# Performance work log

Measured on AMD Instinct MI355X. Metric: run time of the kernel, lower is better.

The kernel has to match this reference:

```python
import jax, jax.numpy as jnp
import numpy as np

B, T, HID = 2, 1024, 2048
H, DK, DV = 16, 128, 128
KC = 4          # short-conv kernel size
CHUNK = 64
EPS = 1e-5


def _dwconv_silu(x, w):
    # causal depthwise conv1d + SiLU: x [B,T,C], w [C,K]
    K = w.shape[1]
    xp = jnp.pad(x, ((0, 0), (K - 1, 0), (0, 0)))
    y = sum(xp[:, i:i + x.shape[1], :] * w[:, i] for i in range(K))
    return jax.nn.silu(y)


def _l2norm(x):
    return x * jax.lax.rsqrt(jnp.sum(x * x, -1, keepdims=True) + 1e-6)


def setup_inputs() -> dict:
    key = jax.random.key(0)
    ks = jax.random.split(key, 22)
    std = 0.02
    w = lambda k, s: jax.random.normal(k, s, jnp.float32) * std
    return dict(
        hidden_states=jax.random.normal(ks[0], (B, T, HID), jnp.float32),
        Wq=w(ks[1], (HID, H * DK)),
        Wk=w(ks[2], (HID, H * DK)),
        Wv=w(ks[3], (HID, H * DV)),
        conv_wq=w(ks[4], (H * DK, KC)),
        conv_wk=w(ks[5], (H * DK, KC)),
        conv_wv=w(ks[6], (H * DV, KC)),
        Wgb1=w(ks[7], (HID, DV)), Wgb2=w(ks[8], (DV, H * DK)),
        Wgd1=w(ks[9], (HID, DV)), Wgd2=w(ks[10], (DV, H * DK)),
        Wbb=w(ks[11], (HID, H)), Wbd=w(ks[12], (HID, H)),
        Wlam=w(ks[13], (HID, H)),
        A_log=jnp.log(jax.random.uniform(ks[14], (H,), jnp.float32, 1.0, 16.0)),
        dt_bias=jnp.zeros((H * DK,), jnp.float32),
        Wg1=w(ks[15], (HID, DV)), Wg2=w(ks[16], (DV, H * DV)),
        bg2=jnp.zeros((H * DV,), jnp.float32),
        onorm_w=jnp.ones((DV,), jnp.float32),
        Wo=w(ks[17], (H * DV, HID)),
    )


def _fkda_core(q, k, v, gf, gs, bf, bs):
    # dual-state (fast/slow) gated delta rule.
    # q,k: [B,T,H,DK]; v: [B,T,H,DV]; gf/gs: log-decay [B,T,H,DK]; bf/bs: [B,T,H]
    scale = DK ** -0.5
    tm = lambda x: jnp.moveaxis(x, 1, 0)                 # time-major
    qT, kT, vT = tm(q) * scale, tm(k), tm(v)
    g2 = jnp.stack([tm(gf), tm(gs)], 1)                  # [T,2,B,H,DK]
    b2 = jnp.stack([tm(bf), tm(bs)], 1)                  # [T,2,B,H]
    NC = T // CHUNK
    chunkify = lambda x: x.reshape((NC, CHUNK) + x.shape[1:])
    inputs = tuple(map(chunkify, (qT, kT, vT, g2, b2)))

    def step(S, inp):
        qt, kt, vt, gt, bt = inp                         # S: [2,B,H,DK,DV]
        S = S * jnp.exp(gt)[..., None]                   # per-channel decay on key dim
        mem = jnp.einsum('bhk,sbhkv->sbhv', kt, S)       # current memory readout
        u = bt[..., None] * (vt[None] - mem)             # delta-rule residual write
        S = S + jnp.einsum('bhk,sbhv->sbhkv', kt, u)
        o = jnp.einsum('bhk,sbhkv->sbhv', qt, S)
        return S, o

    @jax.checkpoint
    def chunk_step(S, inp):
        return jax.lax.scan(step, S, inp)

    S0 = jnp.zeros((2, q.shape[0], H, DK, DV), q.dtype)
    _, o = jax.lax.scan(chunk_step, S0, inputs)          # [NC,CHUNK,2,B,H,DV]
    o = o.reshape((T,) + o.shape[2:])
    return jnp.moveaxis(o[:, 0], 0, 1), jnp.moveaxis(o[:, 1], 0, 1)


def reference(hidden_states, Wq, Wk, Wv, conv_wq, conv_wk, conv_wv,
              Wgb1, Wgb2, Wgd1, Wgd2, Wbb, Wbd, Wlam, A_log, dt_bias,
              Wg1, Wg2, bg2, onorm_w, Wo):
    x = hidden_states
    b, t, _ = x.shape
    q = _dwconv_silu(x @ Wq, conv_wq).reshape(b, t, H, DK)
    k = _dwconv_silu(x @ Wk, conv_wk).reshape(b, t, H, DK)
    v = _dwconv_silu(x @ Wv, conv_wv).reshape(b, t, H, DV)
    g_base = ((x @ Wgb1) @ Wgb2).reshape(b, t, H, DK)    # low-rank decay gates
    g_delta = ((x @ Wgd1) @ Wgd2).reshape(b, t, H, DK)
    bb, bd = x @ Wbb, x @ Wbd
    lam = jax.nn.sigmoid(x @ Wlam)                       # [b,t,H] fast/slow mix
    beta_fast = jax.nn.sigmoid(bb + bd)
    beta_slow = jax.nn.sigmoid(bb - bd)
    dtb = dt_bias.reshape(H, DK)
    gate_of = lambda g: -jnp.exp(A_log)[None, None, :, None] * jax.nn.softplus(g + dtb)
    gf = gate_of(g_base + g_delta)                       # fused_kda_gate, fast
    gs = gate_of(g_base - g_delta)                       # slow (share_decay_gate=False)
    q, k = _l2norm(q), _l2norm(k)                        # use_qk_l2norm_in_kernel
    o_f, o_s = _fkda_core(q, k, v, gf, gs, beta_fast, beta_slow)
    o = lam[..., None] * o_f + (1.0 - lam[..., None]) * o_s
    gate = ((x @ Wg1) @ Wg2 + bg2).reshape(b, t, H, DV)
    o = o * jax.lax.rsqrt(jnp.mean(o * o, -1, keepdims=True) + EPS) * onorm_w
    o = o * jax.nn.sigmoid(gate)                         # FusedRMSNormGated(sigmoid)
    return o.reshape(b, t, H * DV) @ Wo
```

## Files before the change

kernel.cpp:

```cpp
#include <hip/hip_runtime.h>
#include <hip/hip_bf16.h>
#include <math.h>
#include <stdint.h>

#define B_   2
#define T_   1024
#define HID_ 2048
#define H_   16
#define DK_  128
#define DV_  128
#define TS_  16

typedef __bf16 bf16;
typedef __attribute__((ext_vector_type(8))) __bf16 bf16x8;
typedef __attribute__((ext_vector_type(4))) float f32x4;

typedef __attribute__((address_space(3))) uint32_t* lds_ptr_t;
typedef const __attribute__((address_space(1))) uint32_t* glb_ptr_t;

__device__ __forceinline__ float sigmoidf_(float x) {
    return 1.0f / (1.0f + __expf(-x));
}

__device__ __forceinline__ void ldg_to_lds16(const void* g, void* lds) {
    __builtin_amdgcn_global_load_lds((glb_ptr_t)(uintptr_t)g,
                                     (lds_ptr_t)(uintptr_t)lds, 16, 0, 0);
}

template <int CTRL>
__device__ __forceinline__ float dpp_ror_add(float x) {
    int yi = __builtin_amdgcn_update_dpp(
        0, __builtin_bit_cast(int, x), CTRL, 0xF, 0xF, true);
    return x + __builtin_bit_cast(float, yi);
}
__device__ __forceinline__ float row16_allreduce(float x) {
    x = dpp_ror_add<0x128>(x);
    x = dpp_ror_add<0x124>(x);
    x = dpp_ror_add<0x122>(x);
    x = dpp_ror_add<0x121>(x);
    return x;
}

__global__ __launch_bounds__(256) void cast_bf16_kernel(
    const float* __restrict__ in, bf16* __restrict__ out)
{
    int i = blockIdx.x * 256 + threadIdx.x;
    float4 a = ((const float4*)in)[2 * i];
    float4 b = ((const float4*)in)[2 * i + 1];
    bf16x8 o;
    o[0] = (bf16)a.x; o[1] = (bf16)a.y; o[2] = (bf16)a.z; o[3] = (bf16)a.w;
    o[4] = (bf16)b.x; o[5] = (bf16)b.y; o[6] = (bf16)b.z; o[7] = (bf16)b.w;
    ((bf16x8*)out)[i] = o;
}

__global__ __launch_bounds__(256) void tcast_kernel(
    const float* __restrict__ W, bf16* __restrict__ Wt, int K, int N)
{
    __shared__ float tile[32][33];
    const int k0 = blockIdx.y * 32, n0 = blockIdx.x * 32;
    const int r = threadIdx.x >> 5, c = threadIdx.x & 31;
    #pragma unroll
    for (int i = 0; i < 4; ++i)
        tile[r + 8 * i][c] = W[(size_t)(k0 + r + 8 * i) * N + n0 + c];
    __syncthreads();
    #pragma unroll
    for (int i = 0; i < 4; ++i)
        Wt[(size_t)(n0 + r + 8 * i) * K + k0 + c] = (bf16)tile[c][r + 8 * i];
}

__global__ __launch_bounds__(256) void mfma_gemm_kernel(
    const bf16* __restrict__ A, const bf16* __restrict__ Bt,
    const float* __restrict__ bias, void* __restrict__ Cout,
    int M, int N, int Kfull, int lda, int ldc, int ksplit, int bf16out)
{
    __shared__ bf16 As[128 * 32];
    __shared__ bf16 Bs[128 * 32];

    const int tid  = threadIdx.x;
    const int w    = tid >> 6;
    const int lane = tid & 63;
    const int n0   = blockIdx.x * 128;
    const int m0   = blockIdx.y * 128;
    const int wm   = (w >> 1) * 64;
    const int wn   = (w & 1) * 64;

    int kbeg = 0, kend = Kfull;
    float* Cf = (float*)Cout;
    if (ksplit > 0) {
        kbeg = blockIdx.z * ksplit;
        kend = kbeg + ksplit;
        Cf  += (size_t)blockIdx.z * M * N;
    }

    const int lr = lane >> 2;
    const int lc = (lane & 3) * 8;

    f32x4 acc[4][4];
    #pragma unroll
    for (int i = 0; i < 4; ++i)
        #pragma unroll
        for (int j = 0; j < 4; ++j) acc[i][j] = (f32x4)0.0f;

    const bf16* ApL = As + (wm + (lane & 15)) * 32 + (lane >> 4) * 8;
    const bf16* BpL = Bs + (wn + (lane & 15)) * 32 + (lane >> 4) * 8;

    for (int k0 = kbeg; k0 < kend; k0 += 32) {
        #pragma unroll
        for (int i = 0; i < 2; ++i) {
            const int rr = (w * 2 + i) * 16 + lr;
            ldg_to_lds16(A  + (size_t)(m0 + rr) * lda   + k0 + lc, As + (w * 2 + i) * 512);
            ldg_to_lds16(Bt + (size_t)(n0 + rr) * Kfull + k0 + lc, Bs + (w * 2 + i) * 512);
        }
        __syncthreads();

        bf16x8 af[4], bfr[4];
        #pragma unroll
        for (int i = 0; i < 4; ++i) af[i]  = *(const bf16x8*)(ApL + i * 16 * 32);
        #pragma unroll
        for (int j = 0; j < 4; ++j) bfr[j] = *(const bf16x8*)(BpL + j * 16 * 32);
        #pragma unroll
        for (int i = 0; i < 4; ++i)
            #pragma unroll
            for (int j = 0; j < 4; ++j)
                acc[i][j] = __builtin_amdgcn_mfma_f32_16x16x32_bf16(
                    af[i], bfr[j], acc[i][j], 0, 0, 0);
        __syncthreads();
    }

    #pragma unroll
    for (int i = 0; i < 4; ++i) {
        const int row = m0 + wm + i * 16 + (lane >> 4) * 4;
        #pragma unroll
        for (int j = 0; j < 4; ++j) {
            const int col = n0 + wn + j * 16 + (lane & 15);
            const float bv = bias ? bias[col] : 0.0f;
            #pragma unroll
            for (int r = 0; r < 4; ++r) {
                float v = acc[i][j][r] + bv;
                if (bf16out) ((bf16*)Cout)[(size_t)(row + r) * ldc + col] = (bf16)v;
                else         Cf[(size_t)(row + r) * ldc + col] = v;
            }
        }
    }
}

__global__ __launch_bounds__(256) void mid_reduce_kernel(
    const float* __restrict__ midp, bf16* __restrict__ midb)
{
    const size_t plane = (size_t)2048 * 384 / 4;
    size_t i = (size_t)blockIdx.x * 256 + threadIdx.x;
    float4 a = ((const float4*)midp)[i];
    float4 b = ((const float4*)midp)[i + plane];
    float4 c = ((const float4*)midp)[i + 2 * plane];
    float4 d = ((const float4*)midp)[i + 3 * plane];
    float4 s;
    s.x = a.x + b.x + c.x + d.x; s.y = a.y + b.y + c.y + d.y;
    s.z = a.z + b.z + c.z + d.z; s.w = a.w + b.w + c.w + d.w;
    bf16 o[4] = {(bf16)s.x, (bf16)s.y, (bf16)s.z, (bf16)s.w};
    *(uint64_t*)(midb + 4 * i) = *(uint64_t*)o;
}

__global__ __launch_bounds__(256) void skinny3_kernel(
    const float* __restrict__ x, const float* __restrict__ Wbb,
    const float* __restrict__ Wbd, const float* __restrict__ Wlam,
    float* __restrict__ bb, float* __restrict__ bd, float* __restrict__ lam)
{
    __shared__ float xs[16][128];
    __shared__ float wsh[128][48];
    const int m0  = blockIdx.x * 16;
    const int tid = threadIdx.x;
    const int r = tid >> 4, cg = tid & 15;
    float acc0 = 0.f, acc1 = 0.f, acc2 = 0.f;

    for (int k0 = 0; k0 < HID_; k0 += 128) {
        __syncthreads();
        #pragma unroll
        for (int i = 0; i < 2; ++i) {
            int f = tid + 256 * i;
            int rr = f >> 5, cc = (f & 31) * 4;
            *(float4*)&xs[rr][cc] = *(const float4*)(x + (size_t)(m0 + rr) * HID_ + k0 + cc);
        }
        #pragma unroll
        for (int i = 0; i < 2; ++i) {
            int f = tid + 256 * i;
            int kk = f >> 2, cc = (f & 3) * 4;
            *(float4*)&wsh[kk][cc]      = *(const float4*)(Wbb  + (size_t)(k0 + kk) * 16 + cc);
            *(float4*)&wsh[kk][16 + cc] = *(const float4*)(Wbd  + (size_t)(k0 + kk) * 16 + cc);
            *(float4*)&wsh[kk][32 + cc] = *(const float4*)(Wlam + (size_t)(k0 + kk) * 16 + cc);
        }
        __syncthreads();
        #pragma unroll 8
        for (int kk = 0; kk < 128; ++kk) {
            float xv = xs[r][kk];
            acc0 += xv * wsh[kk][cg];
            acc1 += xv * wsh[kk][16 + cg];
            acc2 += xv * wsh[kk][32 + cg];
        }
    }
    size_t o = (size_t)(m0 + r) * 16 + cg;
    bb[o] = acc0; bd[o] = acc1; lam[o] = acc2;
}

__global__ __launch_bounds__(256) void conv_silu_kernel(
    const float* __restrict__ xin, int ldx, int coloff,
    const float* __restrict__ w,
    bf16* __restrict__ ybf, float* __restrict__ yf32, int mode)
{
    const int bt  = blockIdx.x;
    const int t   = bt & (T_ - 1);
    const int tid = threadIdx.x;
    const float* xr = xin + (size_t)bt * ldx + coloff;

    float val[8];
    #pragma unroll
    for (int jj = 0; jj < 8; ++jj) {
        int c = tid + 256 * jj;
        float4 wc = *(const float4*)(w + (size_t)c * 4);
        const float* xc = xr + c;
        float acc = wc.w * xc[0];
        if (t >= 1) acc += wc.z * xc[-ldx];
        if (t >= 2) acc += wc.y * xc[-2 * ldx];
        if (t >= 3) acc += wc.x * xc[-3 * ldx];
        val[jj] = acc * sigmoidf_(acc);
    }

    if (mode > 0) {
        __shared__ float red[4][8];
        const int wv = tid >> 6;
        #pragma unroll
        for (int jj = 0; jj < 8; ++jj) {
            float v2 = val[jj] * val[jj];
            #pragma unroll
            for (int m = 1; m < 64; m <<= 1) v2 += __shfl_xor(v2, m);
            if ((tid & 63) == 0) red[wv][jj] = v2;
        }
        __syncthreads();
        const int wb = (tid >> 7) * 2;
        #pragma unroll
        for (int jj = 0; jj < 8; ++jj) {
            float ss = red[wb][jj] + red[wb + 1][jj];
            float sc = rsqrtf(ss + 1e-6f);
            if (mode == 2) sc *= 0.08838834764831845f;
            val[jj] *= sc;
        }
    }

    const size_t row = (size_t)bt * HID_;
    if (mode == 0) {
        #pragma unroll
        for (int jj = 0; jj < 8; ++jj)
            yf32[row + tid + 256 * jj] = val[jj];
    } else {
        #pragma unroll
        for (int jj = 0; jj < 8; ++jj)
            ybf[row + tid + 256 * jj] = (bf16)val[jj];
    }
}

__global__ __launch_bounds__(256) void decay_gate_kernel(
    float* gb, float* gd,
    const float* __restrict__ A_log, const float* __restrict__ dt_bias)
{
    size_t i = (size_t)blockIdx.x * 256 + threadIdx.x;
    int c = (int)(i & (HID_ - 1));
    int h = c >> 7;
    float a  = gb[i];
    float d  = gd[i];
    float na = -__expf(A_log[h]);
    float db = dt_bias[c];
    float xf = a + d + db;
    float xs = a - d + db;
    float spf = (xf > 20.0f) ? xf : log1pf(__expf(xf));
    float sps = (xs > 20.0f) ? xs : log1pf(__expf(xs));
    gb[i] = __expf(na * spf);
    gd[i] = __expf(na * sps);
}

__global__ __launch_bounds__(256) void fkda_kernel(
    const bf16* __restrict__ qp, const bf16* __restrict__ kp,
    const float* __restrict__ vp, const float* __restrict__ egf,
    const float* __restrict__ egs, const float* __restrict__ bbp,
    const float* __restrict__ bdp,
    float* __restrict__ ofp, float* __restrict__ osp)
{
    const int bx = blockIdx.x;
    const int bh = bx & 31;
    const int sv = bx >> 5;
    const int b  = bh >> 4;
    const int h  = bh & 15;
    const int s  = sv >> 3;
    const int vc = sv & 7;

    const float* eg = s ? egs : egf;
    float*       op = s ? osp : ofp;
    const float  bsign = s ? -1.0f : 1.0f;

    const int tid  = threadIdx.x;
    const int lane = tid & 63;
    const int w    = tid >> 6;
    const int kseg = lane & 15;
    const int colb = w * 4 + (lane >> 4);

    const size_t base = (size_t)b * T_ * HID_ + (size_t)h * DK_;

    __shared__ float EG[TS_ * 128];
    __shared__ bf16  KK[TS_ * 128];
    __shared__ bf16  QQ[TS_ * 128];
    __shared__ float VV[TS_ * 16];
    __shared__ float OT[TS_ * 16];
    __shared__ float BT[TS_];

    float S[8];
    #pragma unroll
    for (int j = 0; j < 8; ++j) S[j] = 0.0f;

    for (int t0 = 0; t0 < T_; t0 += TS_) {
        #pragma unroll
        for (int i = 0; i < 2; ++i) {
            int n = w * 2 + i;
            int f = n * 64 + lane;
            int tt = f >> 5, co = (f & 31) * 4;
            ldg_to_lds16(eg + base + (size_t)(t0 + tt) * HID_ + co, EG + n * 256);
        }
        {
            int f = w * 64 + lane;
            int tt = f >> 4, co = (f & 15) * 8;
            size_t g = base + (size_t)(t0 + tt) * HID_ + co;
            ldg_to_lds16(kp + g, KK + w * 512);
            ldg_to_lds16(qp + g, QQ + w * 512);
        }
        if (tid < 64) {
            int tt = tid >> 2, vo = (tid & 3) * 4;
            size_t g = base + (size_t)(t0 + tt) * HID_ + vc * 16 + vo;
            ((float4*)VV)[tid] = *(const float4*)(vp + g);
        }
        if (tid < TS_) {
            size_t gi = ((size_t)b * T_ + t0 + tid) * H_ + h;
            BT[tid] = sigmoidf_(bbp[gi] + bsign * bdp[gi]);
        }
        __syncthreads();

        for (int tt = 0; tt < TS_; ++tt) {
            float e[8];
            *(float4*)&e[0] = *(const float4*)(EG + tt * 128 + kseg * 8);
            *(float4*)&e[4] = *(const float4*)(EG + tt * 128 + kseg * 8 + 4);
            bf16x8 k8 = *(const bf16x8*)(KK + tt * 128 + kseg * 8);
            bf16x8 q8 = *(const bf16x8*)(QQ + tt * 128 + kseg * 8);
            float vcol = VV[tt * 16 + colb];
            float btv  = BT[tt];

            float kf[8];
            #pragma unroll
            for (int j = 0; j < 8; ++j) kf[j] = (float)k8[j];

            float p0 = 0.0f, p1 = 0.0f;
            #pragma unroll
            for (int j = 0; j < 8; j += 2) {
                S[j]     *= e[j];     p0 += kf[j]     * S[j];
                S[j + 1] *= e[j + 1]; p1 += kf[j + 1] * S[j + 1];
            }
            float p = row16_allreduce(p0 + p1);

            float u = btv * (vcol - p);

            float o0 = 0.0f, o1 = 0.0f;
            #pragma unroll
            for (int j = 0; j < 8; j += 2) {
                S[j]     += kf[j]     * u; o0 += (float)q8[j]     * S[j];
                S[j + 1] += kf[j + 1] * u; o1 += (float)q8[j + 1] * S[j + 1];
            }
            float oo = row16_allreduce(o0 + o1);

            if ((lane & 15) == 0) OT[tt * 16 + colb] = oo;
        }
        __syncthreads();

        if (tid < 64) {
            int tt = tid >> 2, vo = (tid & 3) * 4;
            size_t g = base + (size_t)(t0 + tt) * HID_ + vc * 16 + vo;
            *(float4*)(op + g) = ((const float4*)OT)[tid];
        }
    }
}

__global__ __launch_bounds__(256) void mix_norm_gate_kernel(
    const float* of, const float* os, const float* lam_pre,
    const float* gate, const float* onorm_w, bf16* outp)
{
    const int bt  = blockIdx.x;
    const int tid = threadIdx.x;
    const size_t row = (size_t)bt * HID_;

    float val[8];
    #pragma unroll
    for (int jj = 0; jj < 8; ++jj) {
        int c = tid + 256 * jj;
        int h = c >> 7;
        float l = sigmoidf_(lam_pre[(size_t)bt * H_ + h]);
        val[jj] = l * of[row + c] + (1.0f - l) * os[row + c];
    }

    __shared__ float red[4][8];
    const int wv = tid >> 6;
    #pragma unroll
    for (int jj = 0; jj < 8; ++jj) {
        float v2 = val[jj] * val[jj];
        #pragma unroll
        for (int m = 1; m < 64; m <<= 1) v2 += __shfl_xor(v2, m);
        if ((tid & 63) == 0) red[wv][jj] = v2;
    }
    __syncthreads();
    const int wb = (tid >> 7) * 2;
    #pragma unroll
    for (int jj = 0; jj < 8; ++jj) {
        int c = tid + 256 * jj;
        float ss   = red[wb][jj] + red[wb + 1][jj];
        float mean = ss * (1.0f / 128.0f);
        float sc   = rsqrtf(mean + 1e-5f) * onorm_w[c & 127];
        float g    = sigmoidf_(gate[row + c]);
        outp[row + c] = (bf16)(val[jj] * sc * g);
    }
}

extern "C" void kernel_launch(void* const* d_in, const int* in_sizes, int n_in,
                              void* d_out, int out_size, void* d_ws, size_t ws_size,
                              hipStream_t stream) {
    const float* x       = (const float*)d_in[0];
    const float* Wq      = (const float*)d_in[1];
    const float* Wk      = (const float*)d_in[2];
    const float* Wv      = (const float*)d_in[3];
    const float* conv_wq = (const float*)d_in[4];
    const float* conv_wk = (const float*)d_in[5];
    const float* conv_wv = (const float*)d_in[6];
    const float* Wgb1    = (const float*)d_in[7];
    const float* Wgb2    = (const float*)d_in[8];
    const float* Wgd1    = (const float*)d_in[9];
    const float* Wgd2    = (const float*)d_in[10];
    const float* Wbb     = (const float*)d_in[11];
    const float* Wbd     = (const float*)d_in[12];
    const float* Wlam    = (const float*)d_in[13];
    const float* A_log   = (const float*)d_in[14];
    const float* dt_bias = (const float*)d_in[15];
    const float* Wg1     = (const float*)d_in[16];
    const float* Wg2     = (const float*)d_in[17];
    const float* bg2     = (const float*)d_in[18];
    const float* onorm_w = (const float*)d_in[19];
    const float* Wo      = (const float*)d_in[20];
    float* out = (float*)d_out;

    const size_t M = (size_t)B_ * T_;

    float* ws = (float*)d_ws;
    size_t off = 0;
    auto alloc = [&](size_t nfloats) { float* p = ws + off; off += nfloats; return p; };

    float* bufQKV = alloc(M * 3 * HID_);
    float* wqkvTf = alloc(M * 3 * HID_ / 2);
    float* xbf    = alloc(M * HID_ / 2);
    float* bufQf  = alloc(M * HID_ / 2);
    float* bufKf  = alloc(M * HID_ / 2);
    float* bufV   = alloc(M * HID_);
    float* bufA   = alloc(M * HID_);
    float* bufB   = alloc(M * HID_);
    float* bufC   = alloc(M * HID_);
    float* bufD   = alloc(M * HID_);
    float* bufE   = alloc(M * HID_);
    float* obff   = alloc(M * HID_ / 2);
    float* bb     = alloc(M * H_);
    float* bd     = alloc(M * H_);
    float* lamp   = alloc(M * H_);

    bf16* xb    = (bf16*)xbf;
    bf16* bufQ  = (bf16*)bufQf;
    bf16* bufK  = (bf16*)bufKf;
    bf16* obf   = (bf16*)obff;
    bf16* wqkvT = (bf16*)wqkvTf;
    bf16* wmidT = wqkvT;
    bf16* wexpT = wqkvT + (size_t)384 * HID_;
    bf16* woT   = wqkvT;
    float* midp = bufQKV;
    bf16*  midb = (bf16*)(bufQKV + 4 * M * 384);

    dim3 blk(256);
    auto gemm = [&](const bf16* A, const bf16* Bt, const float* bias, void* C,
                    int Mm, int Nn, int Kk, int lda, int ldc, int ksplit,
                    int bf16out) {
        dim3 grid(Nn / 128, Mm / 128, ksplit ? Kk / ksplit : 1);
        int kf = Kk;
        mfma_gemm_kernel<<<grid, blk, 0, stream>>>(A, Bt, bias, C, Mm, Nn, kf,
                                                   lda, ldc, ksplit, bf16out);
    };
    auto tcast = [&](const float* W, bf16* Wt, int Kk, int Nn) {
        tcast_kernel<<<dim3(Nn / 32, Kk / 32), blk, 0, stream>>>(W, Wt, Kk, Nn);
    };

    cast_bf16_kernel<<<dim3((unsigned)(M * HID_ / 8 / 256)), blk, 0, stream>>>(x, xb);

    tcast(Wq, wqkvT,                         HID_, HID_);
    tcast(Wk, wqkvT + (size_t)HID_ * HID_,   HID_, HID_);
    tcast(Wv, wqkvT + (size_t)2 * HID_ * HID_, HID_, HID_);
    gemm(xb, wqkvT, nullptr, bufQKV, (int)M, 3 * HID_, HID_, HID_, 3 * HID_, 0, 0);

    conv_silu_kernel<<<dim3(B_ * T_), blk, 0, stream>>>(bufQKV, 3 * HID_, 0,
        conv_wq, bufQ, nullptr, 2);
    conv_silu_kernel<<<dim3(B_ * T_), blk, 0, stream>>>(bufQKV, 3 * HID_, HID_,
        conv_wk, bufK, nullptr, 1);
    conv_silu_kernel<<<dim3(B_ * T_), blk, 0, stream>>>(bufQKV, 3 * HID_, 2 * HID_,
        conv_wv, nullptr, bufV, 0);

    skinny3_kernel<<<dim3((unsigned)(M / 16)), blk, 0, stream>>>(
        x, Wbb, Wbd, Wlam, bb, bd, lamp);

    tcast(Wgb1, wmidT,               HID_, DV_);
    tcast(Wgd1, wmidT + HID_ * DV_,  HID_, DV_);
    tcast(Wg1,  wmidT + 2 * HID_ * DV_, HID_, DV_);
    gemm(xb, wmidT, nullptr, midp, (int)M, 384, HID_, HID_, 384, 512, 0);
    mid_reduce_kernel<<<dim3((unsigned)(M * 384 / 4 / 256)), blk, 0, stream>>>(
        midp, midb);

    tcast(Wgb2, wexpT,                   DV_, HID_);
    tcast(Wgd2, wexpT + HID_ * DV_,      DV_, HID_);
    tcast(Wg2,  wexpT + 2 * HID_ * DV_,  DV_, HID_);
    gemm(midb,       wexpT,                  nullptr, bufA, (int)M, HID_, DV_, 384, HID_, 0, 0);
    gemm(midb + 128, wexpT + HID_ * DV_,     nullptr, bufB, (int)M, HID_, DV_, 384, HID_, 0, 0);
    gemm(midb + 256, wexpT + 2 * HID_ * DV_, bg2,     bufE, (int)M, HID_, DV_, 384, HID_, 0, 0);

    decay_gate_kernel<<<dim3((unsigned)(M * HID_ / 256)), blk, 0, stream>>>(
        bufA, bufB, A_log, dt_bias);

    fkda_kernel<<<dim3(512), blk, 0, stream>>>(bufQ, bufK, bufV, bufA, bufB,
                                               bb, bd, bufC, bufD);

    mix_norm_gate_kernel<<<dim3(B_ * T_), blk, 0, stream>>>(
        bufC, bufD, lamp, bufE, onorm_w, obf);

    tcast(Wo, woT, HID_, HID_);
    gemm(obf, woT, nullptr, out, (int)M, HID_, HID_, HID_, HID_, 0, 0);
}
```

Baseline: 778.8 us.

## Fuse gate down-projections into QKV GEMM and fold gate add/sub into weights

Appends the Wgb1/Wgd1/Wg1 down-projections as extra columns of the QKV GEMM (N=6528), which removes the split-K mid GEMM and its reduce kernel. The up-projection is rewritten as one K=256 GEMM against concatenated weights, with Wgd2 negated for the slow half, so it yields g_base±g_delta directly and the decay kernel no longer does the add and subtract. Q and K are now kept in fp32 in the recurrence kernel rather than bf16, with a new lane-to-column mapping for the LDS loads. This trades fewer launches and less intermediate traffic for a larger Q/K memory footprint and more LDS use in the recurrence.

```diff
diff --git a/kernel.cpp b/kernel.cpp
--- a/kernel.cpp
+++ b/kernel.cpp
@@ -68,10 +68,27 @@
         Wt[(size_t)(n0 + r + 8 * i) * K + k0 + c] = (bf16)tile[c][r + 8 * i];
 }
 
+__global__ __launch_bounds__(256) void tcast_off_kernel(
+    const float* __restrict__ W, bf16* __restrict__ Wt,
+    int N, int noff, int koff, float sign)
+{
+    __shared__ float tile[32][33];
+    const int k0 = blockIdx.y * 32, n0 = blockIdx.x * 32;
+    const int r = threadIdx.x >> 5, c = threadIdx.x & 31;
+    #pragma unroll
+    for (int i = 0; i < 4; ++i)
+        tile[r + 8 * i][c] = W[(size_t)(k0 + r + 8 * i) * N + n0 + c];
+    __syncthreads();
+    #pragma unroll
+    for (int i = 0; i < 4; ++i)
+        Wt[(size_t)(noff + n0 + r + 8 * i) * 256 + koff + k0 + c] =
+            (bf16)(sign * tile[c][r + 8 * i]);
+}
+
 __global__ __launch_bounds__(256) void mfma_gemm_kernel(
     const bf16* __restrict__ A, const bf16* __restrict__ Bt,
     const float* __restrict__ bias, void* __restrict__ Cout,
-    int M, int N, int Kfull, int lda, int ldc, int ksplit, int bf16out)
+    int M, int N, int Kfull, int lda, int ldc, int bf16out)
 {
     __shared__ bf16 As[128 * 32];
     __shared__ bf16 Bs[128 * 32];
@@ -84,14 +101,6 @@
     const int wm   = (w >> 1) * 64;
     const int wn   = (w & 1) * 64;
 
-    int kbeg = 0, kend = Kfull;
-    float* Cf = (float*)Cout;
-    if (ksplit > 0) {
-        kbeg = blockIdx.z * ksplit;
-        kend = kbeg + ksplit;
-        Cf  += (size_t)blockIdx.z * M * N;
-    }
-
     const int lr = lane >> 2;
     const int lc = (lane & 3) * 8;
 
@@ -104,7 +113,7 @@
     const bf16* ApL = As + (wm + (lane & 15)) * 32 + (lane >> 4) * 8;
     const bf16* BpL = Bs + (wn + (lane & 15)) * 32 + (lane >> 4) * 8;
 
-    for (int k0 = kbeg; k0 < kend; k0 += 32) {
+    for (int k0 = 0; k0 < Kfull; k0 += 32) {
         #pragma unroll
         for (int i = 0; i < 2; ++i) {
             const int rr = (w * 2 + i) * 16 + lr;
@@ -138,26 +147,20 @@
             for (int r = 0; r < 4; ++r) {
                 float v = acc[i][j][r] + bv;
                 if (bf16out) ((bf16*)Cout)[(size_t)(row + r) * ldc + col] = (bf16)v;
-                else         Cf[(size_t)(row + r) * ldc + col] = v;
+                else ((float*)Cout)[(size_t)(row + r) * ldc + col] = v;
             }
         }
     }
 }
 
-__global__ __launch_bounds__(256) void mid_reduce_kernel(
-    const float* __restrict__ midp, bf16* __restrict__ midb)
-{
-    const size_t plane = (size_t)2048 * 384 / 4;
-    size_t i = (size_t)blockIdx.x * 256 + threadIdx.x;
-    float4 a = ((const float4*)midp)[i];
-    float4 b = ((const float4*)midp)[i + plane];
-    float4 c = ((const float4*)midp)[i + 2 * plane];
-    float4 d = ((const float4*)midp)[i + 3 * plane];
-    float4 s;
-    s.x = a.x + b.x + c.x + d.x; s.y = a.y + b.y + c.y + d.y;
-    s.z = a.z + b.z + c.z + d.z; s.w = a.w + b.w + c.w + d.w;
-    bf16 o[4] = {(bf16)s.x, (bf16)s.y, (bf16)s.z, (bf16)s.w};
-    *(uint64_t*)(midb + 4 * i) = *(uint64_t*)o;
+__global__ __launch_bounds__(256) void midcast_kernel(
+    const float* __restrict__ src, bf16* __restrict__ midb)
+{
+    int i = blockIdx.x * 256 + threadIdx.x;
+    int m = i / 96, c4 = i - m * 96;
+    float4 v = *(const float4*)(src + (size_t)m * 6528 + 6144 + c4 * 4);
+    bf16 o[4] = {(bf16)v.x, (bf16)v.y, (bf16)v.z, (bf16)v.w};
+    *(uint64_t*)(midb + (size_t)m * 384 + c4 * 4) = *(uint64_t*)o;
 }
 
 __global__ __launch_bounds__(256) void skinny3_kernel(
@@ -203,8 +206,7 @@
 
 __global__ __launch_bounds__(256) void conv_silu_kernel(
     const float* __restrict__ xin, int ldx, int coloff,
-    const float* __restrict__ w,
-    bf16* __restrict__ ybf, float* __restrict__ yf32, int mode)
+    const float* __restrict__ w, float* __restrict__ yout, int mode)
 {
     const int bt  = blockIdx.x;
     const int t   = bt & (T_ - 1);
@@ -246,41 +248,36 @@
     }
 
     const size_t row = (size_t)bt * HID_;
-    if (mode == 0) {
-        #pragma unroll
-        for (int jj = 0; jj < 8; ++jj)
-            yf32[row + tid + 256 * jj] = val[jj];
-    } else {
-        #pragma unroll
-        for (int jj = 0; jj < 8; ++jj)
-            ybf[row + tid + 256 * jj] = (bf16)val[jj];
-    }
+    #pragma unroll
+    for (int jj = 0; jj < 8; ++jj)
+        yout[row + tid + 256 * jj] = val[jj];
 }
 
 __global__ __launch_bounds__(256) void decay_gate_kernel(
-    float* gb, float* gd,
-    const float* __restrict__ A_log, const float* __restrict__ dt_bias)
+    float* gfgs, const float* __restrict__ A_log,
+    const float* __restrict__ dt_bias)
 {
     size_t i = (size_t)blockIdx.x * 256 + threadIdx.x;
     int c = (int)(i & (HID_ - 1));
+    size_t m = i >> 11;
     int h = c >> 7;
-    float a  = gb[i];
-    float d  = gd[i];
+    float* pf = gfgs + m * 4096 + c;
+    float* ps = pf + 2048;
     float na = -__expf(A_log[h]);
     float db = dt_bias[c];
-    float xf = a + d + db;
-    float xs = a - d + db;
+    float xf = *pf + db;
+    float xs = *ps + db;
     float spf = (xf > 20.0f) ? xf : log1pf(__expf(xf));
     float sps = (xs > 20.0f) ? xs : log1pf(__expf(xs));
-    gb[i] = __expf(na * spf);
-    gd[i] = __expf(na * sps);
+    *pf = __expf(na * spf);
+    *ps = __expf(na * sps);
 }
 
 __global__ __launch_bounds__(256) void fkda_kernel(
-    const bf16* __restrict__ qp, const bf16* __restrict__ kp,
+    const float* __restrict__ qp, const float* __restrict__ kp,
     const float* __restrict__ vp, const float* __restrict__ egf,
-    const float* __restrict__ egs, const float* __restrict__ bbp,
-    const float* __restrict__ bdp,
+    const float* __restrict__ egs, int ldeg,
+    const float* __restrict__ bbp, const float* __restrict__ bdp,
     float* __restrict__ ofp, float* __restrict__ osp)
 {
     const int bx = blockIdx.x;
@@ -301,11 +298,12 @@
     const int kseg = lane & 15;
     const int colb = w * 4 + (lane >> 4);
 
-    const size_t base = (size_t)b * T_ * HID_ + (size_t)h * DK_;
+    const size_t base  = (size_t)b * T_ * HID_ + (size_t)h * DK_;
+    const size_t baseg = (size_t)b * T_ * ldeg + (size_t)h * DK_;
 
     __shared__ float EG[TS_ * 128];
-    __shared__ bf16  KK[TS_ * 128];
-    __shared__ bf16  QQ[TS_ * 128];
+    __shared__ float KK[TS_ * 128];
+    __shared__ float QQ[TS_ * 128];
     __shared__ float VV[TS_ * 16];
     __shared__ float OT[TS_ * 16];
     __shared__ float BT[TS_];
@@ -314,20 +312,21 @@
     #pragma unroll
     for (int j = 0; j < 8; ++j) S[j] = 0.0f;
 
+    const int l5  = lane & 31;
+    const int ttl = lane >> 5;
+    const int cg  = (l5 < 16) ? (l5 * 8) : ((l5 - 16) * 8 + 4);
+    const int sl  = kseg * 4;
+
     for (int t0 = 0; t0 < T_; t0 += TS_) {
         #pragma unroll
         for (int i = 0; i < 2; ++i) {
-            int n = w * 2 + i;
-            int f = n * 64 + lane;
-            int tt = f >> 5, co = (f & 31) * 4;
-            ldg_to_lds16(eg + base + (size_t)(t0 + tt) * HID_ + co, EG + n * 256);
-        }
-        {
-            int f = w * 64 + lane;
-            int tt = f >> 4, co = (f & 15) * 8;
-            size_t g = base + (size_t)(t0 + tt) * HID_ + co;
-            ldg_to_lds16(kp + g, KK + w * 512);
-            ldg_to_lds16(qp + g, QQ + w * 512);
+            int n  = w * 2 + i;
+            int tt = n * 2 + ttl;
+            size_t rq = base  + (size_t)(t0 + tt) * HID_ + cg;
+            size_t rg = baseg + (size_t)(t0 + tt) * ldeg + cg;
+            ldg_to_lds16(eg + rg, EG + n * 256);
+            ldg_to_lds16(kp + rq, KK + n * 256);
+            ldg_to_lds16(qp + rq, QQ + n * 256);
         }
         if (tid < 64) {
             int tt = tid >> 2, vo = (tid & 3) * 4;
@@ -340,18 +339,17 @@
         }
         __syncthreads();
 
+        #pragma unroll
         for (int tt = 0; tt < TS_; ++tt) {
-            float e[8];
-            *(float4*)&e[0] = *(const float4*)(EG + tt * 128 + kseg * 8);
-            *(float4*)&e[4] = *(const float4*)(EG + tt * 128 + kseg * 8 + 4);
-            bf16x8 k8 = *(const bf16x8*)(KK + tt * 128 + kseg * 8);
-            bf16x8 q8 = *(const bf16x8*)(QQ + tt * 128 + kseg * 8);
+            float e[8], kf[8], qf[8];
+            *(float4*)&e[0]  = *(const float4*)(EG + tt * 128 + sl);
+            *(float4*)&e[4]  = *(const float4*)(EG + tt * 128 + 64 + sl);
+            *(float4*)&kf[0] = *(const float4*)(KK + tt * 128 + sl);
+            *(float4*)&kf[4] = *(const float4*)(KK + tt * 128 + 64 + sl);
+            *(float4*)&qf[0] = *(const float4*)(QQ + tt * 128 + sl);
+            *(float4*)&qf[4] = *(const float4*)(QQ + tt * 128 + 64 + sl);
             float vcol = VV[tt * 16 + colb];
             float btv  = BT[tt];
-
-            float kf[8];
-            #pragma unroll
-            for (int j = 0; j < 8; ++j) kf[j] = (float)k8[j];
 
             float p0 = 0.0f, p1 = 0.0f;
             #pragma unroll
@@ -366,12 +364,12 @@
             float o0 = 0.0f, o1 = 0.0f;
             #pragma unroll
             for (int j = 0; j < 8; j += 2) {
-                S[j]     += kf[j]     * u; o0 += (float)q8[j]     * S[j];
-                S[j + 1] += kf[j + 1] * u; o1 += (float)q8[j + 1] * S[j + 1];
+                S[j]     += kf[j]     * u; o0 += qf[j]     * S[j];
+                S[j + 1] += kf[j + 1] * u; o1 += qf[j + 1] * S[j + 1];
             }
             float oo = row16_allreduce(o0 + o1);
 
-            if ((lane & 15) == 0) OT[tt * 16 + colb] = oo;
+            if (kseg == 0) OT[tt * 16 + colb] = oo;
         }
         __syncthreads();
 
@@ -454,41 +452,35 @@
     size_t off = 0;
     auto alloc = [&](size_t nfloats) { float* p = ws + off; off += nfloats; return p; };
 
-    float* bufQKV = alloc(M * 3 * HID_);
-    float* wqkvTf = alloc(M * 3 * HID_ / 2);
+    float* bufQKV = alloc(M * 6528);
+    float* wqkvTf = alloc((size_t)6528 * HID_ / 2);
     float* xbf    = alloc(M * HID_ / 2);
-    float* bufQf  = alloc(M * HID_ / 2);
-    float* bufKf  = alloc(M * HID_ / 2);
+    float* bufQ   = alloc(M * HID_);
+    float* bufK   = alloc(M * HID_);
     float* bufV   = alloc(M * HID_);
-    float* bufA   = alloc(M * HID_);
-    float* bufB   = alloc(M * HID_);
     float* bufC   = alloc(M * HID_);
     float* bufD   = alloc(M * HID_);
-    float* bufE   = alloc(M * HID_);
-    float* obff   = alloc(M * HID_ / 2);
+    float* midbf  = alloc(M * 384 / 2);
     float* bb     = alloc(M * H_);
     float* bd     = alloc(M * H_);
     float* lamp   = alloc(M * H_);
 
     bf16* xb    = (bf16*)xbf;
-    bf16* bufQ  = (bf16*)bufQf;
-    bf16* bufK  = (bf16*)bufKf;
-    bf16* obf   = (bf16*)obff;
+    bf16* obf   = (bf16*)xbf;
     bf16* wqkvT = (bf16*)wqkvTf;
-    bf16* wmidT = wqkvT;
-    bf16* wexpT = wqkvT + (size_t)384 * HID_;
     bf16* woT   = wqkvT;
-    float* midp = bufQKV;
-    bf16*  midb = (bf16*)(bufQKV + 4 * M * 384);
+    bf16* wcat  = wqkvT + (size_t)HID_ * HID_;
+    bf16* wgate = wcat + (size_t)4096 * 256;
+    bf16* midb  = (bf16*)midbf;
+    float* gfgs = bufQKV;
+    float* bufE = bufQKV + M * 4096;
 
     dim3 blk(256);
     auto gemm = [&](const bf16* A, const bf16* Bt, const float* bias, void* C,
-                    int Mm, int Nn, int Kk, int lda, int ldc, int ksplit,
-                    int bf16out) {
-        dim3 grid(Nn / 128, Mm / 128, ksplit ? Kk / ksplit : 1);
-        int kf = Kk;
-        mfma_gemm_kernel<<<grid, blk, 0, stream>>>(A, Bt, bias, C, Mm, Nn, kf,
-                                                   lda, ldc, ksplit, bf16out);
+                    int Mm, int Nn, int Kk, int lda, int ldc, int bf16out) {
+        dim3 grid(Nn / 128, Mm / 128);
+        mfma_gemm_kernel<<<grid, blk, 0, stream>>>(A, Bt, bias, C, Mm, Nn, Kk,
+                                                   lda, ldc, bf16out);
     };
     auto tcast = [&](const float* W, bf16* Wt, int Kk, int Nn) {
         tcast_kernel<<<dim3(Nn / 32, Kk / 32), blk, 0, stream>>>(W, Wt, Kk, Nn);
@@ -496,44 +488,43 @@
 
     cast_bf16_kernel<<<dim3((unsigned)(M * HID_ / 8 / 256)), blk, 0, stream>>>(x, xb);
 
-    tcast(Wq, wqkvT,                         HID_, HID_);
-    tcast(Wk, wqkvT + (size_t)HID_ * HID_,   HID_, HID_);
-    tcast(Wv, wqkvT + (size_t)2 * HID_ * HID_, HID_, HID_);
-    gemm(xb, wqkvT, nullptr, bufQKV, (int)M, 3 * HID_, HID_, HID_, 3 * HID_, 0, 0);
-
-    conv_silu_kernel<<<dim3(B_ * T_), blk, 0, stream>>>(bufQKV, 3 * HID_, 0,
-        conv_wq, bufQ, nullptr, 2);
-    conv_silu_kernel<<<dim3(B_ * T_), blk, 0, stream>>>(bufQKV, 3 * HID_, HID_,
-        conv_wk, bufK, nullptr, 1);
-    conv_silu_kernel<<<dim3(B_ * T_), blk, 0, stream>>>(bufQKV, 3 * HID_, 2 * HID_,
-        conv_wv, nullptr, bufV, 0);
+    tcast(Wq,   wqkvT,                          HID_, HID_);
+    tcast(Wk,   wqkvT + (size_t)2048 * HID_,    HID_, HID_);
+    tcast(Wv,   wqkvT + (size_t)4096 * HID_,    HID_, HID_);
+    tcast(Wgb1, wqkvT + (size_t)6144 * HID_,    HID_, 128);
+    tcast(Wgd1, wqkvT + (size_t)6272 * HID_,    HID_, 128);
+    tcast(Wg1,  wqkvT + (size_t)6400 * HID_,    HID_, 128);
+    gemm(xb, wqkvT, nullptr, bufQKV, (int)M, 6528, HID_, HID_, 6528, 0);
+
+    conv_silu_kernel<<<dim3(B_ * T_), blk, 0, stream>>>(bufQKV, 6528, 0,
+        conv_wq, bufQ, 2);
+    conv_silu_kernel<<<dim3(B_ * T_), blk, 0, stream>>>(bufQKV, 6528, 2048,
+        conv_wk, bufK, 1);
+    conv_silu_kernel<<<dim3(B_ * T_), blk, 0, stream>>>(bufQKV, 6528, 4096,
+        conv_wv, bufV, 0);
+
+    midcast_kernel<<<dim3((unsigned)(M * 96 / 256)), blk, 0, stream>>>(bufQKV, midb);
 
     skinny3_kernel<<<dim3((unsigned)(M / 16)), blk, 0, stream>>>(
         x, Wbb, Wbd, Wlam, bb, bd, lamp);
 
-    tcast(Wgb1, wmidT,               HID_, DV_);
-    tcast(Wgd1, wmidT + HID_ * DV_,  HID_, DV_);
-    tcast(Wg1,  wmidT + 2 * HID_ * DV_, HID_, DV_);
-    gemm(xb, wmidT, nullptr, midp, (int)M, 384, HID_, HID_, 384, 512, 0);
-    mid_reduce_kernel<<<dim3((unsigned)(M * 384 / 4 / 256)), blk, 0, stream>>>(
-        midp, midb);
-
-    tcast(Wgb2, wexpT,                   DV_, HID_);
-    tcast(Wgd2, wexpT + HID_ * DV_,      DV_, HID_);
-    tcast(Wg2,  wexpT + 2 * HID_ * DV_,  DV_, HID_);
-    gemm(midb,       wexpT,                  nullptr, bufA, (int)M, HID_, DV_, 384, HID_, 0, 0);
-    gemm(midb + 128, wexpT + HID_ * DV_,     nullptr, bufB, (int)M, HID_, DV_, 384, HID_, 0, 0);
-    gemm(midb + 256, wexpT + 2 * HID_ * DV_, bg2,     bufE, (int)M, HID_, DV_, 384, HID_, 0, 0);
+    tcast_off_kernel<<<dim3(64, 4), blk, 0, stream>>>(Wgb2, wcat, HID_, 0,    0,   1.0f);
+    tcast_off_kernel<<<dim3(64, 4), blk, 0, stream>>>(Wgd2, wcat, HID_, 0,    128, 1.0f);
+    tcast_off_kernel<<<dim3(64, 4), blk, 0, stream>>>(Wgb2, wcat, HID_, 2048, 0,   1.0f);
+    tcast_off_kernel<<<dim3(64, 4), blk, 0, stream>>>(Wgd2, wcat, HID_, 2048, 128, -1.0f);
+    tcast(Wg2, wgate, 128, HID_);
+    tcast(Wo,  woT,   HID_, HID_);
+    gemm(midb,       wcat,  nullptr, gfgs, (int)M, 4096, 256, 384, 4096, 0);
+    gemm(midb + 256, wgate, bg2,     bufE, (int)M, HID_, 128, 384, HID_, 0);
 
     decay_gate_kernel<<<dim3((unsigned)(M * HID_ / 256)), blk, 0, stream>>>(
-        bufA, bufB, A_log, dt_bias);
-
-    fkda_kernel<<<dim3(512), blk, 0, stream>>>(bufQ, bufK, bufV, bufA, bufB,
-                                               bb, bd, bufC, bufD);
+        gfgs, A_log, dt_bias);
+
+    fkda_kernel<<<dim3(512), blk, 0, stream>>>(bufQ, bufK, bufV,
+        gfgs, gfgs + 2048, 4096, bb, bd, bufC, bufD);
 
     mix_norm_gate_kernel<<<dim3(B_ * T_), blk, 0, stream>>>(
         bufC, bufD, lamp, bufE, onorm_w, obf);
 
-    tcast(Wo, woT, HID_, HID_);
-    gemm(obf, woT, nullptr, out, (int)M, HID_, HID_, HID_, HID_, 0, 0);
-}
+    gemm(obf, woT, nullptr, out, (int)M, HID_, HID_, HID_, HID_, 0);
+}
```

Result: faster. 751.1 us (-3.6%).
